# Optimization experiments

Hardware: AMD Instinct MI355X
Metric: run time of the kernel (lower is better)

The kernel has to match this reference:

```python
import jax, jax.numpy as jnp
import numpy as np

B, L, D, H = 2, 4096, 1024, 4
DV = D // H
NP = 5
MIN_PROB = 0.01
CHUNK = 32
RIN = D + H * NP * 4 + H * (NP * (NP - 1)) // 2  # 1144
RH = 2 * RIN


def dwconv_causal(x, w):
    # x: (B, L, C); w: (C, K) depthwise causal FIR
    K = w.shape[-1]
    xp = jnp.pad(x, ((0, 0), (K - 1, 0), (0, 0))).transpose(0, 2, 1)  # (B,C,L+K-1)
    y = jax.lax.conv_general_dilated(
        xp, w[:, None, :], window_strides=(1,), padding='VALID',
        feature_group_count=w.shape[0],
        dimension_numbers=('NCH', 'OIH', 'NCH'))
    return y.transpose(0, 2, 1)  # (B,L,C)


def l2norm(x):
    return x * jax.lax.rsqrt(jnp.sum(x * x, -1, keepdims=True) + 1e-12)


def delta_rule_chunkwise(q, k, v, beta, chunk=CHUNK):
    # q,k: (b,h,L,dk)  v: (b,h,L,dv)  beta: (b,h,L); L divisible by chunk
    b, h, Lq, dk = q.shape
    dv = v.shape[-1]
    n = Lq // chunk
    q = l2norm(q); k = l2norm(k)
    v = v * beta[..., None]
    kb = k * beta[..., None]
    r = lambda x: x.reshape(b, h, n, chunk, -1)
    q, k, v, kb = r(q), r(k), r(v), r(kb)
    tri = jnp.triu(jnp.ones((chunk, chunk), bool), 0)
    attn = jnp.where(tri, 0.0, -(kb @ jnp.swapaxes(k, -1, -2)))
    for i in range(1, chunk):  # in-chunk triangular-inverse recurrence
        upd = jnp.einsum('...k,...ki->...i', attn[..., i, :], attn[..., :, :i])
        attn = attn.at[..., i, :i].add(upd)
    attn = attn + jnp.eye(chunk, dtype=attn.dtype)
    u = attn @ v
    w = attn @ kb
    strict = jnp.triu(jnp.ones((chunk, chunk), bool), 1)

    def step(S, inp):
        qi, ki, ui, wi = inp
        la = jnp.where(strict, 0.0, qi @ jnp.swapaxes(ki, -1, -2))
        u_i = ui - wi @ S
        o_i = qi @ S + la @ u_i
        return S + jnp.swapaxes(ki, -1, -2) @ u_i, o_i

    mv = lambda x: jnp.moveaxis(x, 2, 0)
    S0 = jnp.zeros((b, h, dk, dv), q.dtype)
    S, o = jax.lax.scan(step, S0, (mv(q), mv(k), mv(u), mv(w)))
    return jnp.moveaxis(o, 0, 2).reshape(b, h, Lq, dv), S


def setup_inputs() -> dict:
    key = jax.random.key(0)
    ks = jax.random.split(key, 20)
    f = lambda k, shape, s=0.02: jax.random.normal(k, shape, jnp.float32) * s
    # FIR filters: identity tap (last) + small noise, matching learned-from-delta init
    def fir(k, ksz):
        w = np.zeros((D, ksz), np.float32)
        w[:, -1] = 1.0
        return jnp.asarray(w) + f(k, (D, ksz), 0.02)
    b2 = np.zeros((H, NP), np.float32)
    b2[:, -1] = 0.5
    b2[:, -2] = 0.5
    return {
        'hidden_states': jax.random.normal(ks[0], (B, L, D), jnp.float32),
        'Wq': f(ks[1], (D, D)), 'Wk': f(ks[2], (D, D)), 'Wv': f(ks[3], (D, D)),
        'wq_conv': f(ks[4], (D, 4), 0.2), 'wk_conv': f(ks[5], (D, 4), 0.2),
        'wv_conv': f(ks[6], (D, 4), 0.2),
        'Wb': f(ks[7], (H, D)),
        'fir_s_w': fir(ks[8], 3), 'fir_m_w': fir(ks[9], 7),
        'fir_l_w': fir(ks[10], 25), 'fir_id_w': fir(ks[11], 1),
        'W1': f(ks[12], (RH, RIN)), 'b1': jnp.zeros((RH,), jnp.float32),
        'W2': f(ks[13], (H * NP, RH)), 'b2': jnp.asarray(b2.reshape(-1)),
        'norm_w': jnp.ones((DV,), jnp.float32),
        'Wo': f(ks[14], (D, D)),
    }


def reference(hidden_states, Wq, Wk, Wv, wq_conv, wk_conv, wv_conv, Wb,
              fir_s_w, fir_m_w, fir_l_w, fir_id_w, W1, b1, W2, b2, norm_w, Wo):
    silu = jax.nn.silu
    q = silu(dwconv_causal(hidden_states @ Wq.T, wq_conv))
    k = silu(dwconv_causal(hidden_states @ Wk.T, wk_conv))
    v = silu(dwconv_causal(hidden_states @ Wv.T, wv_conv))
    beta = jax.nn.sigmoid(hidden_states @ Wb.T)  # (B,L,H)
    q4 = q.reshape(B, L, H, -1).transpose(0, 2, 1, 3)
    k4 = k.reshape(B, L, H, -1).transpose(0, 2, 1, 3)
    v4 = v.reshape(B, L, H, -1).transpose(0, 2, 1, 3)
    delta_out, _ = delta_rule_chunkwise(q4, k4, v4, beta.transpose(0, 2, 1))
    delta_out = delta_out.transpose(0, 2, 1, 3)  # (B,L,H,DV)
    fir = lambda w: dwconv_causal(v, w).reshape(B, L, H, DV)
    branches = [fir(fir_s_w), fir(fir_m_w), fir(fir_l_w), delta_out, fir(fir_id_w)]
    feats = []
    for x in branches:
        sm = jax.nn.softmax(x, -1)
        feats += [x.mean(-1), jnp.var(x, -1, ddof=1), jnp.max(x, -1),
                  -(sm * jnp.log(sm + 1e-8)).sum(-1)]
    cross = []
    for i in range(NP):
        for j in range(i + 1, NP):
            xi, xj = branches[i], branches[j]
            den = jnp.sqrt(jnp.sum(xi * xi, -1)) * jnp.sqrt(jnp.sum(xj * xj, -1)) + 1e-8
            cross.append(jnp.sum(xi * xj, -1) / den)
    router_in = jnp.concatenate([hidden_states] + feats + cross, axis=-1)  # (B,L,RIN)
    hrt = jax.nn.gelu(router_in @ W1.T + b1, approximate=False)
    logits = (hrt @ W2.T + b2).reshape(B, L, H, NP)
    p = jax.nn.softmax(logits, -1)
    p = p * (1.0 - NP * MIN_PROB) + MIN_PROB  # probability floor
    out = jnp.einsum('blhp,pblhd->blhd', p, jnp.stack(branches))
    out = out * jax.lax.rsqrt(jnp.mean(out * out, -1, keepdims=True) + 1e-5) * norm_w
    return out.reshape(B, L, H * DV) @ Wo.T
```

## Files before the change

### kernel.cpp

```cpp
#include <hip/hip_runtime.h>
#include <stdint.h>

typedef unsigned short u16t;
typedef u16t us4 __attribute__((ext_vector_type(4)));
typedef u16t us8 __attribute__((ext_vector_type(8)));
typedef __bf16 bf8v __attribute__((ext_vector_type(8)));
typedef float f4 __attribute__((ext_vector_type(4)));

#define MFMA(a, b, c) __builtin_amdgcn_mfma_f32_16x16x32_bf16((a), (b), (c), 0, 0, 0)
#define GLOAD_LDS16(g, l) __builtin_amdgcn_global_load_lds( \
    (const __attribute__((address_space(1))) void*)(g),     \
    (__attribute__((address_space(3))) void*)(l), 16, 0, 0)

__device__ __forceinline__ float bf2f(u16t u) {
  union { unsigned int i; float f; } c; c.i = ((unsigned int)u) << 16; return c.f;
}
__device__ __forceinline__ u16t f2bf(float f) {
  union { float f; unsigned int i; } c; c.f = f;
  return (u16t)((c.i + 0x7FFFu + ((c.i >> 16) & 1u)) >> 16);
}
__device__ __forceinline__ float wsum(float v) {
#pragma unroll
  for (int o = 32; o > 0; o >>= 1) v += __shfl_xor(v, o);
  return v;
}
__device__ __forceinline__ float wmax(float v) {
#pragma unroll
  for (int o = 32; o > 0; o >>= 1) v = fmaxf(v, __shfl_xor(v, o));
  return v;
}

__global__ __launch_bounds__(256) void pack_all(const float* __restrict__ hid,
    const float* __restrict__ Wq, const float* __restrict__ Wk, const float* __restrict__ Wv,
    u16t* __restrict__ hidb, u16t* __restrict__ wqb, u16t* __restrict__ wkb,
    u16t* __restrict__ wvb) {
  const int g = blockIdx.x * 256 + threadIdx.x;
  const float* src; u16t* dst; int off;
  if (g < 2097152) { src = hid; dst = hidb; off = g; }
  else if (g < 2359296) { src = Wq; dst = wqb; off = g - 2097152; }
  else if (g < 2621440) { src = Wk; dst = wkb; off = g - 2359296; }
  else { src = Wv; dst = wvb; off = g - 2621440; }
  f4 v = *(const f4*)&src[(size_t)off * 4];
  us4 o;
#pragma unroll
  for (int e = 0; e < 4; ++e) o[e] = f2bf(v[e]);
  *(us4*)&dst[(size_t)off * 4] = o;
}

template <bool CF32, int EPI>
__device__ __forceinline__ void gemm_body(const u16t* __restrict__ A,
    const u16t* __restrict__ Bt, void* __restrict__ Cv, const float* __restrict__ bias,
    int K, int lda, int ldb, int ldc, int m0, int n0) {
  __shared__ u16t As[128][32];
  __shared__ u16t Bs[128][32];
  const int tid = threadIdx.x;
  const int wv = tid >> 6, l = tid & 63;
  const int wr = wv >> 1, wc = wv & 1;
  const int lr = l & 15, kg8 = (l >> 4) * 8, rg4 = (l >> 4) * 4;
  const f4 zf = {0.f, 0.f, 0.f, 0.f};
  f4 acc[4][4];
#pragma unroll
  for (int i = 0; i < 4; ++i)
#pragma unroll
    for (int j = 0; j < 4; ++j) acc[i][j] = zf;

  const u16t* ga = A + (size_t)(m0 + wv * 32 + (l >> 2)) * lda + (l & 3) * 8;
  const u16t* gb = Bt + (size_t)(n0 + wv * 32 + (l >> 2)) * ldb + (l & 3) * 8;
  u16t* la0 = &As[wv * 32][0];
  u16t* la1 = &As[wv * 32 + 16][0];
  u16t* lb0 = &Bs[wv * 32][0];
  u16t* lb1 = &Bs[wv * 32 + 16][0];

  for (int kt = 0; kt < K; kt += 32) {
    GLOAD_LDS16(ga + kt, la0);
    GLOAD_LDS16(ga + (size_t)16 * lda + kt, la1);
    GLOAD_LDS16(gb + kt, lb0);
    GLOAD_LDS16(gb + (size_t)16 * ldb + kt, lb1);
    __syncthreads();
    bf8v af[4], bg[4];
#pragma unroll
    for (int f = 0; f < 4; ++f) af[f] = *(const bf8v*)&As[wr * 64 + f * 16 + lr][kg8];
#pragma unroll
    for (int f = 0; f < 4; ++f) bg[f] = *(const bf8v*)&Bs[wc * 64 + f * 16 + lr][kg8];
#pragma unroll
    for (int i = 0; i < 4; ++i)
#pragma unroll
      for (int j = 0; j < 4; ++j) acc[i][j] = MFMA(af[i], bg[j], acc[i][j]);
    __syncthreads();
  }
#pragma unroll
  for (int i = 0; i < 4; ++i) {
    const int rb = m0 + wr * 64 + i * 16 + rg4;
#pragma unroll
    for (int j = 0; j < 4; ++j) {
      const int cb = n0 + wc * 64 + j * 16 + lr;
#pragma unroll
      for (int r = 0; r < 4; ++r) {
        float x = acc[i][j][r];
        if (EPI == 1) {
          float xx = x + ((cb < 2288) ? bias[cb] : 0.f);
          x = 0.5f * xx * (1.f + erff(xx * 0.70710678118f));
        }
        if (CF32)
          ((float*)Cv)[(size_t)(rb + r) * ldc + cb] = x;
        else
          ((u16t*)Cv)[(size_t)(rb + r) * ldc + cb] = f2bf(x);
      }
    }
  }
}

template <bool CF32, int EPI>
__global__ __launch_bounds__(256) void gemm_bt(const u16t* __restrict__ Av,
    const u16t* __restrict__ Btv, void* __restrict__ Cv, const float* __restrict__ bias,
    int K, int lda, int ldb, int ldc) {
  gemm_body<CF32, EPI>(Av, Btv, Cv, bias, K, lda, ldb, ldc,
                       blockIdx.y * 128, blockIdx.x * 128);
}

__global__ __launch_bounds__(256) void gemm_qkv3(const u16t* __restrict__ A,
    const u16t* __restrict__ B0, const u16t* __restrict__ B1,
    const u16t* __restrict__ B2, u16t* __restrict__ C0, u16t* __restrict__ C1,
    u16t* __restrict__ C2v) {
  const int z = blockIdx.z;
  const u16t* Bt = (z == 0) ? B0 : ((z == 1) ? B1 : B2);
  u16t* C = (z == 0) ? C0 : ((z == 1) ? C1 : C2v);
  gemm_body<false, 0>(A, Bt, C, nullptr, 1024, 1024, 1024, 1024,
                      blockIdx.y * 128, blockIdx.x * 128);
}

__global__ __launch_bounds__(256) void conv4_silu(
    const u16t* __restrict__ qlin, const u16t* __restrict__ klin, const u16t* __restrict__ vlin,
    const float* __restrict__ wq, const float* __restrict__ wk, const float* __restrict__ wvv,
    u16t* __restrict__ qc, u16t* __restrict__ kc, u16t* __restrict__ vc) {
  const int tid = threadIdx.x;
  const int l0 = blockIdx.x * 64;
  const int b = blockIdx.y >> 2, cb = blockIdx.y & 3;
  const int z = blockIdx.z;
  const u16t* in_ = (z == 0) ? qlin : ((z == 1) ? klin : vlin);
  const float* w_ = (z == 0) ? wq : ((z == 1) ? wk : wvv);
  u16t* out_ = (z == 0) ? qc : ((z == 1) ? kc : vc);
  const int c = cb * 256 + tid;
  __shared__ u16t sm[67][256];
  for (int i = 0; i < 67; ++i) {
    int ls = l0 - 3 + i;
    sm[i][tid] = (ls >= 0) ? in_[((size_t)b * 4096 + ls) * 1024 + c] : (u16t)0;
  }
  __syncthreads();
  f4 w4 = *(const f4*)&w_[c * 4];
  float x0 = bf2f(sm[0][tid]), x1 = bf2f(sm[1][tid]), x2 = bf2f(sm[2][tid]);
  for (int ll = 0; ll < 64; ++ll) {
    float x3 = bf2f(sm[ll + 3][tid]);
    float y = x0 * w4[0] + x1 * w4[1] + x2 * w4[2] + x3 * w4[3];
    y = y / (1.f + expf(-y));
    out_[((size_t)b * 4096 + l0 + ll) * 1024 + c] = f2bf(y);
    x0 = x1; x1 = x2; x2 = x3;
  }
}

__global__ __launch_bounds__(256) void prep_kernel(u16t* __restrict__ qc, u16t* __restrict__ kc,
    const u16t* __restrict__ vc, const float* __restrict__ hid, const float* __restrict__ Wb,
    u16t* __restrict__ kbeta, u16t* __restrict__ vbeta) {
  const int m = blockIdx.x, tid = threadIdx.x;
  const int h = tid >> 6, l = tid & 63;
  float bacc = 0.f;
#pragma unroll
  for (int it = 0; it < 4; ++it) {
    int kk = l * 4 + it * 256;
    f4 hv = *(const f4*)&hid[(size_t)m * 1024 + kk];
    f4 wv4 = *(const f4*)&Wb[(size_t)h * 1024 + kk];
#pragma unroll
    for (int e = 0; e < 4; ++e) bacc += hv[e] * wv4[e];
  }
  const float bet = 1.f / (1.f + expf(-wsum(bacc)));
  const size_t base = (size_t)m * 1024 + h * 256 + l * 4;
  us4 q4 = *(const us4*)&qc[base];
  float qf[4]; float ss = 0.f;
#pragma unroll
  for (int e = 0; e < 4; ++e) { qf[e] = bf2f(q4[e]); ss += qf[e] * qf[e]; }
  float qsc = rsqrtf(wsum(ss) + 1e-12f);
  us4 qo;
#pragma unroll
  for (int e = 0; e < 4; ++e) qo[e] = f2bf(qf[e] * qsc);
  *(us4*)&qc[base] = qo;
  us4 k4 = *(const us4*)&kc[base];
  float kf[4]; ss = 0.f;
#pragma unroll
  for (int e = 0; e < 4; ++e) { kf[e] = bf2f(k4[e]); ss += kf[e] * kf[e]; }
  float ksc = rsqrtf(wsum(ss) + 1e-12f);
  us4 ko, kbo;
#pragma unroll
  for (int e = 0; e < 4; ++e) {
    float kn = kf[e] * ksc;
    ko[e] = f2bf(kn);
    kbo[e] = f2bf(kn * bet);
  }
  *(us4*)&kc[base] = ko;
  *(us4*)&kbeta[base] = kbo;
  us4 v4 = *(const us4*)&vc[base];
  us4 vo;
#pragma unroll
  for (int e = 0; e < 4; ++e) vo[e] = f2bf(bf2f(v4[e]) * bet);
  *(us4*)&vbeta[base] = vo;
}

__global__ __launch_bounds__(256) void chunk_uw(const u16t* __restrict__ kn,
    const u16t* __restrict__ kbeta, const u16t* __restrict__ vbeta,
    u16t* __restrict__ ug, u16t* __restrict__ wg) {
  const int tid = threadIdx.x;
  const int bh = blockIdx.x >> 7, ci = blockIdx.x & 127;
  const int b = bh >> 2, h = bh & 3;
  const int l0 = ci * 32;
  __shared__ u16t kns[32][264], kbs[32][264], vbs[32][264];
  __shared__ float attn_s[32][33];
  const int sr = tid >> 5, sd8 = (tid & 31) * 8;
  const size_t rowbase = (size_t)b * 4096 * 1024 + (size_t)h * 256;
#pragma unroll
  for (int i = 0; i < 4; ++i) {
    int r = i * 8 + sr;
    size_t g = rowbase + (size_t)(l0 + r) * 1024 + sd8;
    *(us8*)&kns[r][sd8] = *(const us8*)&kn[g];
    *(us8*)&kbs[r][sd8] = *(const us8*)&kbeta[g];
    *(us8*)&vbs[r][sd8] = *(const us8*)&vbeta[g];
  }
  __syncthreads();
  {
    const int wv = tid >> 6, l = tid & 63;
    const int lr = l & 15, kg8 = (l >> 4) * 8, rg4 = (l >> 4) * 4;
    const int rq = wv >> 1, rk = wv & 1;
    f4 t4 = {0.f, 0.f, 0.f, 0.f};
#pragma unroll
    for (int ks = 0; ks < 8; ++ks) {
      bf8v a = *(const bf8v*)&kbs[rq * 16 + lr][ks * 32 + kg8];
      bf8v bb = *(const bf8v*)&kns[rk * 16 + lr][ks * 32 + kg8];
      t4 = MFMA(a, bb, t4);
    }
    const int colj = rk * 16 + lr;
#pragma unroll
    for (int rr = 0; rr < 4; ++rr) {
      const int rowr = rq * 16 + rg4 + rr;
      attn_s[rowr][colj] = (colj < rowr) ? -t4[rr] : 0.f;
    }
  }
  __syncthreads();
  if (tid < 32) {
    const int j = tid;
    for (int i = 1; i < 32; ++i) {
      float aij = attn_s[i][j];
      float upd = 0.f;
#pragma unroll 1
      for (int k = 1; k < 31; ++k) {
        float aik = __shfl(aij, k);
        float akj = (k > j && k < i) ? attn_s[k][j] : 0.f;
        upd += aik * akj;
      }
      if (j < i) attn_s[i][j] = aij + upd;
    }
    attn_s[j][j] = 1.f;
  }
  __syncthreads();
  {
    const int r = tid >> 3, cg = (tid & 7) * 32;
    float ua[32], wa[32];
#pragma unroll
    for (int e = 0; e < 32; ++e) { ua[e] = 0.f; wa[e] = 0.f; }
    for (int j = 0; j < 32; ++j) {
      float a = attn_s[r][j];
#pragma unroll
      for (int e0 = 0; e0 < 32; e0 += 8) {
        us8 v8 = *(const us8*)&vbs[j][cg + e0];
        us8 k8 = *(const us8*)&kbs[j][cg + e0];
#pragma unroll
        for (int e = 0; e < 8; ++e) {
          ua[e0 + e] += a * bf2f(v8[e]);
          wa[e0 + e] += a * bf2f(k8[e]);
        }
      }
    }
    const size_t ob = ((size_t)bh * 4096 + l0 + r) * 256 + cg;
#pragma unroll
    for (int e0 = 0; e0 < 32; e0 += 8) {
      us8 pu, pw;
#pragma unroll
      for (int e = 0; e < 8; ++e) { pu[e] = f2bf(ua[e0 + e]); pw[e] = f2bf(wa[e0 + e]); }
      *(us8*)&ug[ob + e0] = pu;
      *(us8*)&wg[ob + e0] = pw;
    }
  }
}

__global__ __launch_bounds__(256, 1) void delta_scan(const u16t* __restrict__ qn,
    const u16t* __restrict__ kn, const u16t* __restrict__ ug, const u16t* __restrict__ wg,
    u16t* __restrict__ dout, const u16t* __restrict__ vc, const float* __restrict__ w25g,
    u16t* __restrict__ fl, const float* __restrict__ W1, u16t* __restrict__ W1p,
    const float* __restrict__ Wo, u16t* __restrict__ wob) {
  const int blk = blockIdx.x;
  const int tid = threadIdx.x;
  if (blk < 32) {
    const int bh = blk >> 2, vbidx = blk & 3;
    const int b = bh >> 2, h = bh & 3;
    const int c0 = vbidx * 64;
    const int wv = tid >> 6, l = tid & 63;
    const int lr = l & 15, kg8 = (l >> 4) * 8, rg4 = (l >> 4) * 4;

    __shared__ u16t qs[32][264], ks2[32][264], wss[32][264];
    __shared__ u16t kts[256][40];
    __shared__ u16t sbf[64][264];
    __shared__ u16t las[32][40];
    __shared__ u16t uts[64][40];

    {
      u16t* sp = &sbf[0][0];
      for (int i = tid; i < 64 * 264; i += 256) sp[i] = 0;
    }
    const f4 zf = {0.f, 0.f, 0.f, 0.f};
    f4 sacc[16];
#pragma unroll
    for (int d = 0; d < 16; ++d) sacc[d] = zf;
    __syncthreads();

    const u16t* qb = qn + (size_t)b * 4096 * 1024 + (size_t)h * 256;
    const u16t* knb = kn + (size_t)b * 4096 * 1024 + (size_t)h * 256;
    const u16t* ub = ug + (size_t)bh * 4096 * 256;
    const u16t* wb = wg + (size_t)bh * 4096 * 256;
    const int sr = tid >> 5, sd8 = (tid & 31) * 8;

    us8 pq[4], pk[4], pw[4];
    us4 pu0, pu1;
#pragma unroll
    for (int i = 0; i < 4; ++i) {
      const int r = i * 8 + sr;
      pq[i] = *(const us8*)(qb + (size_t)r * 1024 + sd8);
      pk[i] = *(const us8*)(knb + (size_t)r * 1024 + sd8);
      pw[i] = *(const us8*)(wb + (size_t)r * 256 + sd8);
    }
    pu0 = *(const us4*)(ub + (size_t)lr * 256 + c0 + wv * 16 + rg4);
    pu1 = *(const us4*)(ub + (size_t)(16 + lr) * 256 + c0 + wv * 16 + rg4);

    for (int ci = 0; ci < 128; ++ci) {
      const int l0 = ci * 32;
#pragma unroll
      for (int i = 0; i < 4; ++i) {
        const int r = i * 8 + sr;
        *(us8*)&qs[r][sd8] = pq[i];
        *(us8*)&ks2[r][sd8] = pk[i];
        *(us8*)&wss[r][sd8] = pw[i];
      }
      const us4 u0 = pu0, u1 = pu1;
      __syncthreads();
      if (ci < 127) {
        const int l1 = l0 + 32;
#pragma unroll
        for (int i = 0; i < 4; ++i) {
          const int r = i * 8 + sr;
          pq[i] = *(const us8*)(qb + (size_t)(l1 + r) * 1024 + sd8);
          pk[i] = *(const us8*)(knb + (size_t)(l1 + r) * 1024 + sd8);
          pw[i] = *(const us8*)(wb + (size_t)(l1 + r) * 256 + sd8);
        }
        pu0 = *(const us4*)(ub + (size_t)(l1 + lr) * 256 + c0 + wv * 16 + rg4);
        pu1 = *(const us4*)(ub + (size_t)(l1 + 16 + lr) * 256 + c0 + wv * 16 + rg4);
      }
      {
        const int dk = tid;
        const int swz = ((dk >> 3) & 3) << 3;
#pragma unroll
        for (int r = 0; r < 32; r += 2) {
          unsigned int lo = ks2[r][dk], hi = ks2[r + 1][dk];
          *(unsigned int*)&kts[dk][r ^ swz] = lo | (hi << 16);
        }
      }
      {
        const int rq = wv >> 1, rk = wv & 1;
        f4 t4 = zf;
#pragma unroll
        for (int ks = 0; ks < 8; ++ks) {
          bf8v a = *(const bf8v*)&qs[rq * 16 + lr][ks * 32 + kg8];
          bf8v bb = *(const bf8v*)&ks2[rk * 16 + lr][ks * 32 + kg8];
          t4 = MFMA(a, bb, t4);
        }
        const int colj = rk * 16 + lr;
#pragma unroll
        for (int rr = 0; rr < 4; ++rr) {
          const int rowr = rq * 16 + rg4 + rr;
          las[rowr][colj] = (colj <= rowr) ? f2bf(t4[rr]) : (u16t)0;
        }
      }
      f4 o0 = zf, o1 = zf;
      {
        f4 m0 = zf, m1 = zf;
#pragma unroll
        for (int ks = 0; ks < 8; ++ks) {
          bf8v a = *(const bf8v*)&sbf[wv * 16 + lr][ks * 32 + kg8];
          bf8v wb0 = *(const bf8v*)&wss[lr][ks * 32 + kg8];
          bf8v wb1 = *(const bf8v*)&wss[16 + lr][ks * 32 + kg8];
          bf8v qb0 = *(const bf8v*)&qs[lr][ks * 32 + kg8];
          bf8v qb1 = *(const bf8v*)&qs[16 + lr][ks * 32 + kg8];
          m0 = MFMA(a, wb0, m0);
          m1 = MFMA(a, wb1, m1);
          o0 = MFMA(a, qb0, o0);
          o1 = MFMA(a, qb1, o1);
        }
#pragma unroll
        for (int rt = 0; rt < 2; ++rt) {
          f4 mm = rt ? m1 : m0;
          const us4 uu = rt ? u1 : u0;
          const int r = rt * 16 + lr;
#pragma unroll
          for (int rr = 0; rr < 4; ++rr)
            uts[wv * 16 + rg4 + rr][r] = f2bf(bf2f(uu[rr]) - mm[rr]);
        }
      }
      __syncthreads();
      {
        bf8v a2 = *(const bf8v*)&uts[wv * 16 + lr][kg8];
        {
          bf8v lb0 = *(const bf8v*)&las[lr][kg8];
          bf8v lb1 = *(const bf8v*)&las[16 + lr][kg8];
          o0 = MFMA(a2, lb0, o0);
          o1 = MFMA(a2, lb1, o1);
        }
#pragma unroll
        for (int rt = 0; rt < 2; ++rt) {
          f4 oo = rt ? o1 : o0;
          const int r = rt * 16 + lr;
          us4 st;
#pragma unroll
          for (int rr = 0; rr < 4; ++rr) st[rr] = f2bf(oo[rr]);
          *(us4*)(dout + ((size_t)(b * 4096 + l0 + r) * 4 + h) * 256 + c0 + wv * 16 + rg4) = st;
        }
#pragma unroll
        for (int d = 0; d < 16; ++d) {
          const int swzd = ((2 * d + (lr >> 3)) & 3) << 3;
          bf8v bb = *(const bf8v*)&kts[d * 16 + lr][kg8 ^ swzd];
          sacc[d] = MFMA(a2, bb, sacc[d]);
        }
#pragma unroll
        for (int d = 0; d < 16; ++d) {
#pragma unroll
          for (int rr = 0; rr < 4; ++rr)
            sbf[wv * 16 + rg4 + rr][d * 16 + lr] = f2bf(sacc[d][rr]);
        }
      }
      __syncthreads();
    }
    return;
  }
  if (blk < 544) {
    const int fb = blk - 32;
    const int l0 = (fb & 63) * 64;
    const int by = fb >> 6;
    const int b = by >> 2, cb = by & 3;
    const int c = cb * 256 + tid;
    __shared__ u16t sm[88][256];
    for (int i = 0; i < 88; ++i) {
      int ls = l0 - 24 + i;
      sm[i][tid] = (ls >= 0) ? vc[((size_t)b * 4096 + ls) * 1024 + c] : (u16t)0;
    }
    __syncthreads();
    float w25[25];
#pragma unroll
    for (int j = 0; j < 25; ++j) w25[j] = w25g[c * 25 + j];
    float x[25];
#pragma unroll
    for (int j = 0; j < 25; ++j) x[j] = bf2f(sm[j][tid]);
    for (int ll = 0; ll < 64; ++ll) {
      float yl = 0.f;
#pragma unroll
      for (int j = 0; j < 25; ++j) yl += x[j] * w25[j];
      fl[((size_t)b * 4096 + l0 + ll) * 1024 + c] = f2bf(yl);
      if (ll < 63) {
#pragma unroll
        for (int j = 0; j < 24; ++j) x[j] = x[j + 1];
        x[24] = bf2f(sm[ll + 25][tid]);
      }
    }
    return;
  }
  if (blk < 672) {
    for (size_t idx = (size_t)(blk - 544) * 256 + tid; idx < (size_t)2304 * 1152;
         idx += (size_t)128 * 256) {
      int n = (int)(idx / 1152), k = (int)(idx % 1152);
      W1p[idx] = (n < 2288 && k < 1144) ? f2bf(W1[(size_t)n * 1144 + k]) : (u16t)0;
    }
    return;
  }
  for (size_t i = (size_t)(blk - 672) * 256 + tid; i < 262144; i += (size_t)64 * 256) {
    f4 v = *(const f4*)&Wo[i * 4];
    us4 o;
#pragma unroll
    for (int e = 0; e < 4; ++e) o[e] = f2bf(v[e]);
    *(us4*)&wob[i * 4] = o;
  }
}

__device__ __forceinline__ void fir_otf(const u16t* __restrict__ vc,
    const float* __restrict__ w3g, const float* __restrict__ w7g,
    const float* __restrict__ w1g, int b, int lseq, int c0,
    float ys[4], float ym[4], float yi[4]) {
  float xs[7][4];
#pragma unroll
  for (int j = 0; j < 7; ++j) {
    int ls = lseq - 6 + j;
    if (ls >= 0) {
      us4 v = *(const us4*)&vc[((size_t)b * 4096 + ls) * 1024 + c0];
#pragma unroll
      for (int e = 0; e < 4; ++e) xs[j][e] = bf2f(v[e]);
    } else {
#pragma unroll
      for (int e = 0; e < 4; ++e) xs[j][e] = 0.f;
    }
  }
#pragma unroll
  for (int e = 0; e < 4; ++e) {
    const int c = c0 + e;
    ys[e] = xs[4][e] * w3g[c * 3] + xs[5][e] * w3g[c * 3 + 1] + xs[6][e] * w3g[c * 3 + 2];
    float m_ = 0.f;
#pragma unroll
    for (int j = 0; j < 7; ++j) m_ += xs[j][e] * w7g[c * 7 + j];
    ym[e] = m_;
    yi[e] = xs[6][e] * w1g[c];
  }
}

__global__ __launch_bounds__(256) void features_kernel(const float* __restrict__ hid,
    const u16t* __restrict__ vc, const float* __restrict__ w3g, const float* __restrict__ w7g,
    const float* __restrict__ w1g, const u16t* __restrict__ fl, const u16t* __restrict__ dlt,
    u16t* __restrict__ router) {
  const int m = blockIdx.x, tid = threadIdx.x;
  const int h = tid >> 6, l = tid & 63;
  const int b = m >> 12, lseq = m & 4095;
  const int c0 = h * 256 + l * 4;
  const size_t base = (size_t)m * 1024 + c0;
  float x[5][4];
  fir_otf(vc, w3g, w7g, w1g, b, lseq, c0, x[0], x[1], x[4]);
  {
    us4 v2 = *(const us4*)&fl[base];
    us4 v3 = *(const us4*)&dlt[base];
#pragma unroll
    for (int e = 0; e < 4; ++e) { x[2][e] = bf2f(v2[e]); x[3][e] = bf2f(v3[e]); }
  }
  float s1[5], s2[5], mx[5];
#pragma unroll
  for (int br = 0; br < 5; ++br) {
    float a = 0.f, bq = 0.f, m_ = -1e30f;
#pragma unroll
    for (int e = 0; e < 4; ++e) {
      a += x[br][e]; bq += x[br][e] * x[br][e]; m_ = fmaxf(m_, x[br][e]);
    }
    s1[br] = wsum(a); s2[br] = wsum(bq); mx[br] = wmax(m_);
  }
  float ent[5];
#pragma unroll
  for (int br = 0; br < 5; ++br) {
    float e_ = 0.f;
#pragma unroll
    for (int e = 0; e < 4; ++e) e_ += expf(x[br][e] - mx[br]);
    float es = wsum(e_);
    float hn = 0.f;
#pragma unroll
    for (int e = 0; e < 4; ++e) {
      float pv = expf(x[br][e] - mx[br]) / es;
      hn += pv * logf(pv + 1e-8f);
    }
    ent[br] = -wsum(hn);
  }
  float dt[10];
  {
    int pi = 0;
#pragma unroll
    for (int i = 0; i < 5; ++i)
#pragma unroll
      for (int j = i + 1; j < 5; ++j) {
        float d = 0.f;
#pragma unroll
        for (int e = 0; e < 4; ++e) d += x[i][e] * x[j][e];
        dt[pi] = wsum(d);
        ++pi;
      }
  }
  if (l == 0) {
    u16t* rp = router + (size_t)m * 1152 + 1024;
#pragma unroll
    for (int br = 0; br < 5; ++br) {
      float mean = s1[br] * (1.f / 256.f);
      float var = (s2[br] - s1[br] * s1[br] * (1.f / 256.f)) * (1.f / 255.f);
      rp[br * 16 + 0 + h] = f2bf(mean);
      rp[br * 16 + 4 + h] = f2bf(var);
      rp[br * 16 + 8 + h] = f2bf(mx[br]);
      rp[br * 16 + 12 + h] = f2bf(ent[br]);
    }
    int pi = 0;
#pragma unroll
    for (int i = 0; i < 5; ++i)
#pragma unroll
      for (int j = i + 1; j < 5; ++j) {
        float den = sqrtf(s2[i]) * sqrtf(s2[j]) + 1e-8f;
        rp[80 + pi * 4 + h] = f2bf(dt[pi] / den);
        ++pi;
      }
  }
  {
    f4 hv = *(const f4*)&hid[(size_t)m * 1024 + tid * 4];
    us4 hv4;
#pragma unroll
    for (int e = 0; e < 4; ++e) hv4[e] = f2bf(hv[e]);
    *(us4*)&router[(size_t)m * 1152 + tid * 4] = hv4;
  }
  if (tid < 8) router[(size_t)m * 1152 + 1144 + tid] = 0;
}

__global__ __launch_bounds__(256) void route_mix(const u16t* __restrict__ hrt,
    const float* __restrict__ W2, const float* __restrict__ b2,
    const u16t* __restrict__ vc, const float* __restrict__ w3g,
    const float* __restrict__ w7g, const float* __restrict__ w1g,
    const u16t* __restrict__ fl, const u16t* __restrict__ dlt,
    const float* __restrict__ normw, u16t* __restrict__ mixed) {
  const int m = blockIdx.x, tid = threadIdx.x;
  const int h = tid >> 6, l = tid & 63;
  float acc[5];
#pragma unroll
  for (int n = 0; n < 5; ++n) acc[n] = 0.f;
  for (int kk = l * 4; kk < 2288; kk += 256) {
    us4 hv = *(const us4*)&hrt[(size_t)m * 2304 + kk];
    float hf[4];
#pragma unroll
    for (int e = 0; e < 4; ++e) hf[e] = bf2f(hv[e]);
#pragma unroll
    for (int n = 0; n < 5; ++n) {
      f4 wv4 = *(const f4*)&W2[(size_t)(h * 5 + n) * 2288 + kk];
#pragma unroll
      for (int e = 0; e < 4; ++e) acc[n] += hf[e] * wv4[e];
    }
  }
  float p5[5];
  {
    float lg[5];
#pragma unroll
    for (int n = 0; n < 5; ++n) lg[n] = wsum(acc[n]) + b2[h * 5 + n];
    float mxv = lg[0];
#pragma unroll
    for (int n = 1; n < 5; ++n) mxv = fmaxf(mxv, lg[n]);
    float es = 0.f, ev[5];
#pragma unroll
    for (int n = 0; n < 5; ++n) { ev[n] = expf(lg[n] - mxv); es += ev[n]; }
#pragma unroll
    for (int n = 0; n < 5; ++n) p5[n] = (ev[n] / es) * 0.95f + 0.01f;
  }
  const int b = m >> 12, lseq = m & 4095;
  const int c0 = h * 256 + l * 4;
  const size_t base = (size_t)m * 1024 + c0;
  float x[5][4];
  fir_otf(vc, w3g, w7g, w1g, b, lseq, c0, x[0], x[1], x[4]);
  {
    us4 v2 = *(const us4*)&fl[base];
    us4 v3 = *(const us4*)&dlt[base];
#pragma unroll
    for (int e = 0; e < 4; ++e) { x[2][e] = bf2f(v2[e]); x[3][e] = bf2f(v3[e]); }
  }
  float o[4] = {0.f, 0.f, 0.f, 0.f};
#pragma unroll
  for (int br = 0; br < 5; ++br)
#pragma unroll
    for (int e = 0; e < 4; ++e) o[e] += p5[br] * x[br][e];
  float ss = 0.f;
#pragma unroll
  for (int e = 0; e < 4; ++e) ss += o[e] * o[e];
  ss = wsum(ss);
  float sc = rsqrtf(ss * (1.f / 256.f) + 1e-5f);
  f4 nw = *(const f4*)&normw[l * 4];
  us4 ov;
#pragma unroll
  for (int e = 0; e < 4; ++e) ov[e] = f2bf(o[e] * sc * nw[e]);
  *(us4*)&mixed[base] = ov;
}

extern "C" void kernel_launch(void* const* d_in, const int* in_sizes, int n_in,
                              void* d_out, int out_size, void* d_ws, size_t ws_size,
                              hipStream_t stream) {
  (void)in_sizes; (void)n_in; (void)out_size; (void)ws_size;
  const float* hid = (const float*)d_in[0];
  const float* Wq = (const float*)d_in[1];
  const float* Wk = (const float*)d_in[2];
  const float* Wv = (const float*)d_in[3];
  const float* wqc = (const float*)d_in[4];
  const float* wkc = (const float*)d_in[5];
  const float* wvc = (const float*)d_in[6];
  const float* Wb = (const float*)d_in[7];
  const float* fsw = (const float*)d_in[8];
  const float* fmw = (const float*)d_in[9];
  const float* flw = (const float*)d_in[10];
  const float* fiw = (const float*)d_in[11];
  const float* W1 = (const float*)d_in[12];
  const float* b1 = (const float*)d_in[13];
  const float* W2 = (const float*)d_in[14];
  const float* b2 = (const float*)d_in[15];
  const float* nwt = (const float*)d_in[16];
  const float* Wo = (const float*)d_in[17];
  float* out = (float*)d_out;

  char* wsp = (char*)d_ws;
  const size_t S = (size_t)2 * 4096 * 1024 * 2;
  u16t* ql = (u16t*)(wsp + 0 * S);
  u16t* kl = (u16t*)(wsp + 1 * S);
  u16t* vl = (u16t*)(wsp + 2 * S);
  u16t* qc = (u16t*)(wsp + 3 * S);
  u16t* kc = (u16t*)(wsp + 4 * S);
  u16t* vc = (u16t*)(wsp + 5 * S);
  u16t* ubuf = (u16t*)(wsp + 6 * S);
  u16t* wbuf = (u16t*)(wsp + 7 * S);
  char* p = wsp + 8 * S;
  u16t* router = (u16t*)p; p += (size_t)8192 * 1152 * 2;
  u16t* hrt = (u16t*)p;    p += (size_t)8192 * 2304 * 2;
  u16t* w1p = (u16t*)p;    p += (size_t)2304 * 1152 * 2;
  u16t* wob = (u16t*)p;    p += (size_t)1024 * 1024 * 2;
  u16t* hidb = qc;
  u16t* wqb = kc;
  u16t* wkb = kc + 1048576;
  u16t* wvb = kc + 2097152;
  u16t* kbeta = ql;
  u16t* vbeta = kl;
  u16t* dlt = kl;
  u16t* f_l = vl;
  u16t* mixed = wbuf;

  dim3 blk(256);
  pack_all<<<dim3(11264), blk, 0, stream>>>(hid, Wq, Wk, Wv, hidb, wqb, wkb, wvb);
  gemm_qkv3<<<dim3(8, 64, 3), blk, 0, stream>>>(hidb, wqb, wkb, wvb, ql, kl, vl);
  conv4_silu<<<dim3(64, 8, 3), blk, 0, stream>>>(ql, kl, vl, wqc, wkc, wvc, qc, kc, vc);
  prep_kernel<<<dim3(8192), blk, 0, stream>>>(qc, kc, vc, hid, Wb, kbeta, vbeta);
  chunk_uw<<<dim3(1024), blk, 0, stream>>>(kc, kbeta, vbeta, ubuf, wbuf);
  delta_scan<<<dim3(736), blk, 0, stream>>>(qc, kc, ubuf, wbuf, dlt, vc, flw, f_l,
                                            W1, w1p, Wo, wob);
  features_kernel<<<dim3(8192), blk, 0, stream>>>(hid, vc, fsw, fmw, fiw, f_l, dlt, router);
  gemm_bt<false, 1><<<dim3(18, 64), blk, 0, stream>>>(router, w1p, hrt, b1, 1152, 1152, 1152, 2304);
  route_mix<<<dim3(8192), blk, 0, stream>>>(hrt, W2, b2, vc, fsw, fmw, fiw, f_l, dlt, nwt, mixed);
  gemm_bt<true, 0><<<dim3(8, 64), blk, 0, stream>>>(mixed, wob, out, nullptr, 1024, 1024, 1024, 1024);
}
```

Baseline: 1.039 ms.

## Move router logits projection to MFMA GEMM and transpose FIR weights

Replaces the per-row scalar W2 dot products in route_mix with a separate small MFMA GEMM over hrt and a bf16, zero-padded copy of W2. The GEMM writes fp32 logits that route_mix then reads. FIR filter weights are transposed to channel-contiguous layouts in pack_all so fir_otf can load them as float4 vectors instead of strided scalars. This adds a kernel launch and a logits buffer, and W2 is now rounded to bf16, which slightly changes precision. The logits GEMM runs on only 64 blocks.

```diff
diff --git a/kernel.cpp b/kernel.cpp
--- a/kernel.cpp
+++ b/kernel.cpp
@@ -32,19 +32,32 @@
 
 __global__ __launch_bounds__(256) void pack_all(const float* __restrict__ hid,
     const float* __restrict__ Wq, const float* __restrict__ Wk, const float* __restrict__ Wv,
+    const float* __restrict__ fsw, const float* __restrict__ fmw,
     u16t* __restrict__ hidb, u16t* __restrict__ wqb, u16t* __restrict__ wkb,
-    u16t* __restrict__ wvb) {
+    u16t* __restrict__ wvb, float* __restrict__ w3t, float* __restrict__ w7t) {
   const int g = blockIdx.x * 256 + threadIdx.x;
-  const float* src; u16t* dst; int off;
-  if (g < 2097152) { src = hid; dst = hidb; off = g; }
-  else if (g < 2359296) { src = Wq; dst = wqb; off = g - 2097152; }
-  else if (g < 2621440) { src = Wk; dst = wkb; off = g - 2359296; }
-  else { src = Wv; dst = wvb; off = g - 2621440; }
-  f4 v = *(const f4*)&src[(size_t)off * 4];
-  us4 o;
-#pragma unroll
-  for (int e = 0; e < 4; ++e) o[e] = f2bf(v[e]);
-  *(us4*)&dst[(size_t)off * 4] = o;
+  if (g < 2883584) {
+    const float* src; u16t* dst; int off;
+    if (g < 2097152) { src = hid; dst = hidb; off = g; }
+    else if (g < 2359296) { src = Wq; dst = wqb; off = g - 2097152; }
+    else if (g < 2621440) { src = Wk; dst = wkb; off = g - 2359296; }
+    else { src = Wv; dst = wvb; off = g - 2621440; }
+    f4 v = *(const f4*)&src[(size_t)off * 4];
+    us4 o;
+#pragma unroll
+    for (int e = 0; e < 4; ++e) o[e] = f2bf(v[e]);
+    *(us4*)&dst[(size_t)off * 4] = o;
+    return;
+  }
+  int idx = g - 2883584;
+  if (idx < 3072) {
+    int j = idx >> 10, c = idx & 1023;
+    w3t[idx] = fsw[c * 3 + j];
+  } else if (idx < 10240) {
+    int idx2 = idx - 3072;
+    int j = idx2 / 1024, c = idx2 & 1023;
+    w7t[idx2] = fmw[c * 7 + j];
+  }
 }
 
 template <bool CF32, int EPI>
@@ -127,6 +140,61 @@
   u16t* C = (z == 0) ? C0 : ((z == 1) ? C1 : C2v);
   gemm_body<false, 0>(A, Bt, C, nullptr, 1024, 1024, 1024, 1024,
                       blockIdx.y * 128, blockIdx.x * 128);
+}
+
+__global__ __launch_bounds__(256) void logits_gemm(const u16t* __restrict__ hrt,
+    const u16t* __restrict__ W2b, const float* __restrict__ b2, float* __restrict__ logits) {
+  __shared__ u16t As[128][32];
+  __shared__ u16t Bs[32][32];
+  const int tid = threadIdx.x;
+  const int wv = tid >> 6, l = tid & 63;
+  const int lr = l & 15, kg8 = (l >> 4) * 8, rg4 = (l >> 4) * 4;
+  const int m0 = blockIdx.x * 128;
+  const f4 zf = {0.f, 0.f, 0.f, 0.f};
+  f4 acc[2][2];
+#pragma unroll
+  for (int i = 0; i < 2; ++i)
+#pragma unroll
+    for (int j = 0; j < 2; ++j) acc[i][j] = zf;
+
+  const u16t* ga = hrt + (size_t)(m0 + wv * 32 + (l >> 2)) * 2304 + (l & 3) * 8;
+  const u16t* gb = W2b + (size_t)(l >> 2) * 2304 + (l & 3) * 8;
+  u16t* la0 = &As[wv * 32][0];
+  u16t* la1 = &As[wv * 32 + 16][0];
+
+  for (int kt = 0; kt < 2304; kt += 32) {
+    GLOAD_LDS16(ga + kt, la0);
+    GLOAD_LDS16(ga + (size_t)16 * 2304 + kt, la1);
+    if (wv == 0) {
+      GLOAD_LDS16(gb + kt, &Bs[0][0]);
+      GLOAD_LDS16(gb + (size_t)16 * 2304 + kt, &Bs[16][0]);
+    }
+    __syncthreads();
+    bf8v af[2], bg[2];
+#pragma unroll
+    for (int f = 0; f < 2; ++f) af[f] = *(const bf8v*)&As[wv * 32 + f * 16 + lr][kg8];
+#pragma unroll
+    for (int f = 0; f < 2; ++f) bg[f] = *(const bf8v*)&Bs[f * 16 + lr][kg8];
+#pragma unroll
+    for (int i = 0; i < 2; ++i)
+#pragma unroll
+      for (int j = 0; j < 2; ++j) acc[i][j] = MFMA(af[i], bg[j], acc[i][j]);
+    __syncthreads();
+  }
+#pragma unroll
+  for (int i = 0; i < 2; ++i) {
+    const int rb = m0 + wv * 32 + i * 16 + rg4;
+#pragma unroll
+    for (int j = 0; j < 2; ++j) {
+      const int cb = j * 16 + lr;
+#pragma unroll
+      for (int r = 0; r < 4; ++r) {
+        float x = acc[i][j][r];
+        if (cb < 20) x += b2[cb];
+        logits[(size_t)(rb + r) * 32 + cb] = x;
+      }
+    }
+  }
 }
 
 __global__ __launch_bounds__(256) void conv4_silu(
@@ -293,7 +361,8 @@
     const u16t* __restrict__ kn, const u16t* __restrict__ ug, const u16t* __restrict__ wg,
     u16t* __restrict__ dout, const u16t* __restrict__ vc, const float* __restrict__ w25g,
     u16t* __restrict__ fl, const float* __restrict__ W1, u16t* __restrict__ W1p,
-    const float* __restrict__ Wo, u16t* __restrict__ wob) {
+    const float* __restrict__ Wo, u16t* __restrict__ wob, const float* __restrict__ W2,
+    u16t* __restrict__ W2b) {
   const int blk = blockIdx.x;
   const int tid = threadIdx.x;
   if (blk < 32) {
@@ -484,17 +553,25 @@
     }
     return;
   }
-  for (size_t i = (size_t)(blk - 672) * 256 + tid; i < 262144; i += (size_t)64 * 256) {
-    f4 v = *(const f4*)&Wo[i * 4];
-    us4 o;
-#pragma unroll
-    for (int e = 0; e < 4; ++e) o[e] = f2bf(v[e]);
-    *(us4*)&wob[i * 4] = o;
+  if (blk < 736) {
+    for (size_t i = (size_t)(blk - 672) * 256 + tid; i < 262144; i += (size_t)64 * 256) {
+      f4 v = *(const f4*)&Wo[i * 4];
+      us4 o;
+#pragma unroll
+      for (int e = 0; e < 4; ++e) o[e] = f2bf(v[e]);
+      *(us4*)&wob[i * 4] = o;
+    }
+    return;
+  }
+  for (size_t idx = (size_t)(blk - 736) * 256 + tid; idx < (size_t)32 * 2304;
+       idx += (size_t)16 * 256) {
+    int n = (int)(idx / 2304), k = (int)(idx % 2304);
+    W2b[idx] = (n < 20 && k < 2288) ? f2bf(W2[(size_t)n * 2288 + k]) : (u16t)0;
   }
 }
 
 __device__ __forceinline__ void fir_otf(const u16t* __restrict__ vc,
-    const float* __restrict__ w3g, const float* __restrict__ w7g,
+    const float* __restrict__ w3t, const float* __restrict__ w7t,
     const float* __restrict__ w1g, int b, int lseq, int c0,
     float ys[4], float ym[4], float yi[4]) {
   float xs[7][4];
@@ -510,20 +587,25 @@
       for (int e = 0; e < 4; ++e) xs[j][e] = 0.f;
     }
   }
+  f4 w3v[3], w7v[7], w1v;
+#pragma unroll
+  for (int j = 0; j < 3; ++j) w3v[j] = *(const f4*)&w3t[j * 1024 + c0];
+#pragma unroll
+  for (int j = 0; j < 7; ++j) w7v[j] = *(const f4*)&w7t[j * 1024 + c0];
+  w1v = *(const f4*)&w1g[c0];
 #pragma unroll
   for (int e = 0; e < 4; ++e) {
-    const int c = c0 + e;
-    ys[e] = xs[4][e] * w3g[c * 3] + xs[5][e] * w3g[c * 3 + 1] + xs[6][e] * w3g[c * 3 + 2];
+    ys[e] = xs[4][e] * w3v[0][e] + xs[5][e] * w3v[1][e] + xs[6][e] * w3v[2][e];
     float m_ = 0.f;
 #pragma unroll
-    for (int j = 0; j < 7; ++j) m_ += xs[j][e] * w7g[c * 7 + j];
+    for (int j = 0; j < 7; ++j) m_ += xs[j][e] * w7v[j][e];
     ym[e] = m_;
-    yi[e] = xs[6][e] * w1g[c];
+    yi[e] = xs[6][e] * w1v[e];
   }
 }
 
 __global__ __launch_bounds__(256) void features_kernel(const float* __restrict__ hid,
-    const u16t* __restrict__ vc, const float* __restrict__ w3g, const float* __restrict__ w7g,
+    const u16t* __restrict__ vc, const float* __restrict__ w3t, const float* __restrict__ w7t,
     const float* __restrict__ w1g, const u16t* __restrict__ fl, const u16t* __restrict__ dlt,
     u16t* __restrict__ router) {
   const int m = blockIdx.x, tid = threadIdx.x;
@@ -532,7 +614,7 @@
   const int c0 = h * 256 + l * 4;
   const size_t base = (size_t)m * 1024 + c0;
   float x[5][4];
-  fir_otf(vc, w3g, w7g, w1g, b, lseq, c0, x[0], x[1], x[4]);
+  fir_otf(vc, w3t, w7t, w1g, b, lseq, c0, x[0], x[1], x[4]);
   {
     us4 v2 = *(const us4*)&fl[base];
     us4 v3 = *(const us4*)&dlt[base];
@@ -609,34 +691,18 @@
   if (tid < 8) router[(size_t)m * 1152 + 1144 + tid] = 0;
 }
 
-__global__ __launch_bounds__(256) void route_mix(const u16t* __restrict__ hrt,
-    const float* __restrict__ W2, const float* __restrict__ b2,
-    const u16t* __restrict__ vc, const float* __restrict__ w3g,
-    const float* __restrict__ w7g, const float* __restrict__ w1g,
+__global__ __launch_bounds__(256) void route_mix(const float* __restrict__ logits,
+    const u16t* __restrict__ vc, const float* __restrict__ w3t,
+    const float* __restrict__ w7t, const float* __restrict__ w1g,
     const u16t* __restrict__ fl, const u16t* __restrict__ dlt,
     const float* __restrict__ normw, u16t* __restrict__ mixed) {
   const int m = blockIdx.x, tid = threadIdx.x;
   const int h = tid >> 6, l = tid & 63;
-  float acc[5];
-#pragma unroll
-  for (int n = 0; n < 5; ++n) acc[n] = 0.f;
-  for (int kk = l * 4; kk < 2288; kk += 256) {
-    us4 hv = *(const us4*)&hrt[(size_t)m * 2304 + kk];
-    float hf[4];
-#pragma unroll
-    for (int e = 0; e < 4; ++e) hf[e] = bf2f(hv[e]);
-#pragma unroll
-    for (int n = 0; n < 5; ++n) {
-      f4 wv4 = *(const f4*)&W2[(size_t)(h * 5 + n) * 2288 + kk];
-#pragma unroll
-      for (int e = 0; e < 4; ++e) acc[n] += hf[e] * wv4[e];
-    }
-  }
   float p5[5];
   {
     float lg[5];
 #pragma unroll
-    for (int n = 0; n < 5; ++n) lg[n] = wsum(acc[n]) + b2[h * 5 + n];
+    for (int n = 0; n < 5; ++n) lg[n] = logits[(size_t)m * 32 + h * 5 + n];
     float mxv = lg[0];
 #pragma unroll
     for (int n = 1; n < 5; ++n) mxv = fmaxf(mxv, lg[n]);
@@ -650,7 +716,7 @@
   const int c0 = h * 256 + l * 4;
   const size_t base = (size_t)m * 1024 + c0;
   float x[5][4];
-  fir_otf(vc, w3g, w7g, w1g, b, lseq, c0, x[0], x[1], x[4]);
+  fir_otf(vc, w3t, w7t, w1g, b, lseq, c0, x[0], x[1], x[4]);
   {
     us4 v2 = *(const us4*)&fl[base];
     us4 v3 = *(const us4*)&dlt[base];
@@ -713,6 +779,10 @@
   u16t* hrt = (u16t*)p;    p += (size_t)8192 * 2304 * 2;
   u16t* w1p = (u16t*)p;    p += (size_t)2304 * 1152 * 2;
   u16t* wob = (u16t*)p;    p += (size_t)1024 * 1024 * 2;
+  u16t* w2b = (u16t*)p;    p += (size_t)32 * 2304 * 2;
+  float* logits = (float*)p; p += (size_t)8192 * 32 * 4;
+  float* w3t = (float*)p;  p += (size_t)3 * 1024 * 4;
+  float* w7t = (float*)p;  p += (size_t)7 * 1024 * 4;
   u16t* hidb = qc;
   u16t* wqb = kc;
   u16t* wkb = kc + 1048576;
@@ -724,15 +794,17 @@
   u16t* mixed = wbuf;
 
   dim3 blk(256);
-  pack_all<<<dim3(11264), blk, 0, stream>>>(hid, Wq, Wk, Wv, hidb, wqb, wkb, wvb);
+  pack_all<<<dim3(11304), blk, 0, stream>>>(hid, Wq, Wk, Wv, fsw, fmw,
+                                            hidb, wqb, wkb, wvb, w3t, w7t);
   gemm_qkv3<<<dim3(8, 64, 3), blk, 0, stream>>>(hidb, wqb, wkb, wvb, ql, kl, vl);
   conv4_silu<<<dim3(64, 8, 3), blk, 0, stream>>>(ql, kl, vl, wqc, wkc, wvc, qc, kc, vc);
   prep_kernel<<<dim3(8192), blk, 0, stream>>>(qc, kc, vc, hid, Wb, kbeta, vbeta);
   chunk_uw<<<dim3(1024), blk, 0, stream>>>(kc, kbeta, vbeta, ubuf, wbuf);
-  delta_scan<<<dim3(736), blk, 0, stream>>>(qc, kc, ubuf, wbuf, dlt, vc, flw, f_l,
-                                            W1, w1p, Wo, wob);
-  features_kernel<<<dim3(8192), blk, 0, stream>>>(hid, vc, fsw, fmw, fiw, f_l, dlt, router);
+  delta_scan<<<dim3(752), blk, 0, stream>>>(qc, kc, ubuf, wbuf, dlt, vc, flw, f_l,
+                                            W1, w1p, Wo, wob, W2, w2b);
+  features_kernel<<<dim3(8192), blk, 0, stream>>>(hid, vc, w3t, w7t, fiw, f_l, dlt, router);
   gemm_bt<false, 1><<<dim3(18, 64), blk, 0, stream>>>(router, w1p, hrt, b1, 1152, 1152, 1152, 2304);
-  route_mix<<<dim3(8192), blk, 0, stream>>>(hrt, W2, b2, vc, fsw, fmw, fiw, f_l, dlt, nwt, mixed);
+  logits_gemm<<<dim3(64), blk, 0, stream>>>(hrt, w2b, b2, logits);
+  route_mix<<<dim3(8192), blk, 0, stream>>>(logits, vc, w3t, w7t, fiw, f_l, dlt, nwt, mixed);
   gemm_bt<true, 0><<<dim3(8, 64), blk, 0, stream>>>(mixed, wob, out, nullptr, 1024, 1024, 1024, 1024);
 }
```

Result: faster. 992.4 us (-4.5%).
